# Performance work log

Hardware: AMD Instinct MI355X
Metric: run time of the kernel (lower is better)

Reference implementation:

```python
import jax, jax.numpy as jnp
import numpy as np

B, L, D, N = 32, 512, 512, 8  # batch, length, input_size, num_labels


def setup_inputs() -> dict:
    key = jax.random.key(0)
    k1, k2, k3, k4, k5 = jax.random.split(key, 5)
    scale = 0.02
    return {
        "input_h": jax.random.normal(k1, (B, L, D), dtype=jnp.float32),
        "input_c": jax.random.normal(k2, (B, L, D), dtype=jnp.float32),
        "mask": jnp.ones((B, L), dtype=jnp.float32),
        "U": jax.random.normal(k3, (N, D, D), dtype=jnp.float32) * scale,
        "W_d": jax.random.normal(k4, (N, D), dtype=jnp.float32) * scale,
        "W_e": jax.random.normal(k5, (N, D), dtype=jnp.float32) * scale,
        "b": jnp.zeros((N, 1, 1), dtype=jnp.float32),
    }


def reference(input_h, input_c, mask, U, W_d, W_e, b):
    # Biaffine attention (NeuroNLP2 BiAAttention): head = decoder side, child = encoder side.
    # bilinear term: [b, n, l_head, l_child]
    out = jnp.einsum("bld,nde,bme->bnlm", input_h, U, input_c)
    # linear head term -> broadcast over child axis
    out = out + jnp.einsum("nd,bld->bnl", W_d, input_h)[:, :, :, None]
    # linear child term -> broadcast over head axis
    out = out + jnp.einsum("nd,bmd->bnm", W_e, input_c)[:, :, None, :]
    out = out + b[None]  # bias [n,1,1]
    # mask_d / mask_e multiplicative masking
    out = out * mask[:, None, :, None] * mask[:, None, None, :]
    # -inf on the diagonal (no self-arcs)
    length = out.shape[-1]
    diag = jnp.where(jnp.eye(length, dtype=bool), -jnp.inf, 0.0).astype(out.dtype)
    return out + diag
```

## Files before the change

kernel.cpp:

```cpp
#include <hip/hip_runtime.h>


#define B_ 32
#define L_ 512
#define D_ 512
#define N_ 8
#define MT 64
#define STR 536

using f16x8 = __attribute__((ext_vector_type(8))) _Float16;
using f32x4 = __attribute__((ext_vector_type(4))) float;
using u16x8 = __attribute__((ext_vector_type(8))) unsigned short;

static __device__ __forceinline__ float bf2f(unsigned short h) {
  union { unsigned u; float f; } v; v.u = (unsigned)h << 16; return v.f;
}
static __device__ __forceinline__ float h2f(unsigned short h) {
  _Float16 x; __builtin_memcpy(&x, &h, 2); return (float)x;
}
static __device__ __forceinline__ unsigned short f2h(float f) {
  _Float16 x = (_Float16)f; unsigned short u; __builtin_memcpy(&u, &x, 2); return u;
}

static __device__ __forceinline__ int sniff(const unsigned* mkw) {
  const unsigned w = *mkw;
  if (w == 0x3F800000u) return 0;
  if (w == 0x3C003C00u) return 1;
  if (w == 0x3F803F80u) return 2;
  return 1;
}

static __device__ __forceinline__ float ldscal(const void* base, int idx, int flag) {
  if (flag == 0) return ((const float*)base)[idx];
  const unsigned short u = ((const unsigned short*)base)[idx];
  return (flag == 1) ? h2f(u) : bf2f(u);
}

static __device__ __forceinline__ u16x8 ld8f(const void* base, size_t off, int flag) {
  u16x8 o;
  if (flag == 1) {
    o = *(const u16x8*)((const unsigned short*)base + off);
  } else if (flag == 0) {
    const float4* p = (const float4*)((const float*)base + off);
    float4 a = p[0], bq = p[1];
    o[0]=f2h(a.x); o[1]=f2h(a.y); o[2]=f2h(a.z); o[3]=f2h(a.w);
    o[4]=f2h(bq.x); o[5]=f2h(bq.y); o[6]=f2h(bq.z); o[7]=f2h(bq.w);
  } else {
    u16x8 v = *(const u16x8*)((const unsigned short*)base + off);
#pragma unroll
    for (int j = 0; j < 8; ++j) o[j] = f2h(bf2f(v[j]));
  }
  return o;
}

__global__ __launch_bounds__(256)
void cvt_f16(const void* __restrict__ src, unsigned short* __restrict__ dst, int n8,
             const unsigned* __restrict__ mkw) {
  const int flag = sniff(mkw);
  int i = blockIdx.x * 256 + threadIdx.x;
  const int stride = gridDim.x * 256;
  for (; i < n8; i += stride) {
    u16x8 o = ld8f(src, 8 * (size_t)i, flag);
    *(u16x8*)(dst + 8 * (size_t)i) = o;
  }
}

__global__ __launch_bounds__(256)
void cvt_f16_2(const void* __restrict__ s0, unsigned short* __restrict__ d0, int n0,
               const void* __restrict__ s1, unsigned short* __restrict__ d1, int n1,
               const unsigned* __restrict__ mkw) {
  const int flag = sniff(mkw);
  int i = blockIdx.x * 256 + threadIdx.x;
  const int stride = gridDim.x * 256;
  const int tot = n0 + n1;
  for (; i < tot; i += stride) {
    const void* src; unsigned short* dst; int k;
    if (i < n0) { src = s0; dst = d0; k = i; }
    else        { src = s1; dst = d1; k = i - n0; }
    u16x8 o = ld8f(src, 8 * (size_t)k, flag);
    *(u16x8*)(dst + 8 * (size_t)k) = o;
  }
}

__global__ __launch_bounds__(256)
void prep_c(const void* __restrict__ Cr, unsigned short* __restrict__ Cc,
            float* __restrict__ CTp, const void* __restrict__ We,
            const void* __restrict__ Bia, const unsigned* __restrict__ mkw)
{
  __shared__ float wetab[N_ * 512];
  __shared__ float psum[256 * 9];
  const int flag = sniff(mkw);
  const int tid = threadIdx.x;
  const int b  = blockIdx.x >> 4;
  const int mc = blockIdx.x & 15;

  for (int i = tid; i < N_ * 512; i += 256) wetab[i] = ldscal(We, i, flag);
  __syncthreads();

  const int ml = tid >> 3;
  const int e8 = tid & 7;
  const int m  = mc * 32 + ml;
  const size_t rowOff = ((size_t)b * L_ + m) * D_;

  float pn[N_];
#pragma unroll
  for (int nn = 0; nn < N_; ++nn) pn[nn] = 0.f;

#pragma unroll
  for (int j = 0; j < 8; ++j) {
    const int e0 = (j * 8 + e8) * 8;
    u16x8 v = ld8f(Cr, rowOff + e0, flag);
    *(u16x8*)(Cc + rowOff + e0) = v;
    float cf[8];
#pragma unroll
    for (int k = 0; k < 8; ++k) cf[k] = h2f(v[k]);
#pragma unroll
    for (int nn = 0; nn < N_; ++nn) {
      float s = pn[nn];
#pragma unroll
      for (int k = 0; k < 8; ++k) s += cf[k] * wetab[nn * 512 + e0 + k];
      pn[nn] = s;
    }
  }
#pragma unroll
  for (int nn = 0; nn < N_; ++nn) psum[tid * 9 + nn] = pn[nn];
  __syncthreads();

  {
    const int row = tid >> 3, nn = tid & 7;
    float s = ldscal(Bia, nn, flag);
#pragma unroll
    for (int q = 0; q < 8; ++q) s += psum[(row * 8 + q) * 9 + nn];
    CTp[((size_t)(b * N_ + nn)) * L_ + mc * 32 + row] = s;
  }
}

template <bool CVT, bool CT>
__global__ __launch_bounds__(512)
void biaffine(const unsigned short* __restrict__ Hc, const void* __restrict__ Hr,
              const unsigned short* __restrict__ Cc, const void* __restrict__ Cr,
              const unsigned short* __restrict__ Uc, const void* __restrict__ Ur,
              const float* __restrict__ CTp,
              const void* __restrict__ Mk, const void* __restrict__ Wd,
              const void* __restrict__ We, const void* __restrict__ Bia,
              unsigned short* __restrict__ Out)
{
  __shared__ __align__(16) unsigned short cpb[64 * STR];
  __shared__ float wdv[512], mlv[512];
  __shared__ float wev[512], psum[512];
  __shared__ float colterm[64], mcv[64];

  const int flag = sniff((const unsigned*)Mk);
  const int tid  = threadIdx.x;
  const int wave = tid >> 6;
  const int lane = tid & 63;
  const int quad = lane >> 4;
  const int l16  = lane & 15;

  const int bid = blockIdx.x;
  const int n  = bid & 7;
  const int mt = (bid >> 3) & 7;
  const int b  = bid >> 6;

  const size_t cOff = ((size_t)b * L_ + mt * MT) * D_;
  const size_t hOff = (size_t)b * L_ * D_;
  const size_t uOff = (size_t)n * D_ * D_;

  auto ld8 = [&](const void* base, size_t off) -> u16x8 { return ld8f(base, off, flag); };

  size_t uo[4];
#pragma unroll
  for (int di = 0; di < 4; ++di)
    uo[di] = uOff + (size_t)((4 * wave + di) * 16 + l16) * D_ + quad * 8;

  auto ldU = [&](int di, int s) -> f16x8 {
    if constexpr (CVT) { u16x8 t = ld8(Ur, uo[di] + (size_t)s * 32); return *(f16x8*)&t; }
    else               return *(const f16x8*)(Uc + uo[di] + (size_t)s * 32);
  };

  f16x8 bB[2][4];
#pragma unroll
  for (int di = 0; di < 4; ++di) bB[0][di] = ldU(di, 0);

  {
    const int row = tid >> 3, cb0 = (tid & 7) * 64;
    u16x8 t[8];
#pragma unroll
    for (int j = 0; j < 8; ++j) {
      if constexpr (CVT) t[j] = ld8(Cr, cOff + (size_t)row * D_ + cb0 + j * 8);
      else               t[j] = ((const u16x8*)(Cc + cOff + (size_t)row * D_ + cb0))[j];
    }
    u16x8* dst = (u16x8*)&cpb[row * STR + cb0];
#pragma unroll
    for (int j = 0; j < 8; ++j) dst[j] = t[j];
  }
  wdv[tid] = ldscal(Wd, n * D_ + tid, flag);
  mlv[tid] = ldscal(Mk, b * L_ + tid, flag);
  if (tid < 64) mcv[tid] = ldscal(Mk, b * L_ + mt * MT + tid, flag);
  if constexpr (CT) {
    if (tid < 64) colterm[tid] = CTp[((size_t)(b * N_ + n)) * L_ + mt * MT + tid];
  } else {
    wev[tid] = ldscal(We, n * D_ + tid, flag);
  }
  __syncthreads();

  if constexpr (!CT) {
    {
      const int m = tid >> 3, e0 = (tid & 7) * 64;
      float s = 0.f;
#pragma unroll 8
      for (int e = 0; e < 64; ++e) s += h2f(cpb[m * STR + e0 + e]) * wev[e0 + e];
      psum[tid] = s;
    }
    __syncthreads();
    if (tid < 64) {
      float s = ldscal(Bia, n, flag);
#pragma unroll
      for (int j = 0; j < 8; ++j) s += psum[tid * 8 + j];
      colterm[tid] = s;
    }
  }

  f32x4 acc[4][4];
#pragma unroll
  for (int i = 0; i < 4; ++i)
#pragma unroll
    for (int j = 0; j < 4; ++j) acc[i][j] = (f32x4){0.f, 0.f, 0.f, 0.f};

#pragma unroll
  for (int s = 0; s < 16; ++s) {
    const int cur = s & 1;
    if (s < 15) {
#pragma unroll
      for (int di = 0; di < 4; ++di) bB[cur ^ 1][di] = ldU(di, s + 1);
    }
    f16x8 aF[4];
#pragma unroll
    for (int mi = 0; mi < 4; ++mi)
      aF[mi] = *(const f16x8*)&cpb[(mi * 16 + l16) * STR + s * 32 + quad * 8];
    __builtin_amdgcn_s_setprio(1);
#pragma unroll
    for (int mi = 0; mi < 4; ++mi)
#pragma unroll
      for (int di = 0; di < 4; ++di)
        acc[mi][di] = __builtin_amdgcn_mfma_f32_16x16x32_f16(aF[mi], bB[cur][di], acc[mi][di], 0, 0, 0);
    __builtin_amdgcn_s_setprio(0);
  }

  size_t ho[4];
#pragma unroll
  for (int li = 0; li < 4; ++li)
    ho[li] = hOff + (size_t)((4 * wave + li) * 16 + l16) * D_ + quad * 8;

  auto ldH = [&](int li, int s) -> f16x8 {
    if constexpr (CVT) { u16x8 t = ld8(Hr, ho[li] + (size_t)s * 32); return *(f16x8*)&t; }
    else               return *(const f16x8*)(Hc + ho[li] + (size_t)s * 32);
  };

  f16x8 aB[2][4];
#pragma unroll
  for (int li = 0; li < 4; ++li) aB[0][li] = ldH(li, 0);

  __syncthreads();

#pragma unroll
  for (int di = 0; di < 4; ++di) {
    const int d_g = (4 * wave + di) * 16 + l16;
    const float wd = wdv[d_g];
#pragma unroll
    for (int mi = 0; mi < 4; ++mi)
#pragma unroll
      for (int r = 0; r < 4; ++r) {
        const int m_loc = mi * 16 + quad * 4 + r;
        cpb[m_loc * STR + d_g] = f2h(acc[mi][di][r] + wd);
      }
  }
  __syncthreads();

  f32x4 acc2[4][4];
#pragma unroll
  for (int i = 0; i < 4; ++i)
#pragma unroll
    for (int j = 0; j < 4; ++j) acc2[i][j] = (f32x4){0.f, 0.f, 0.f, 0.f};

#pragma unroll
  for (int s = 0; s < 16; ++s) {
    const int cur = s & 1;
    if (s < 15) {
#pragma unroll
      for (int li = 0; li < 4; ++li) aB[cur ^ 1][li] = ldH(li, s + 1);
    }
    f16x8 bF[4];
#pragma unroll
    for (int mj = 0; mj < 4; ++mj)
      bF[mj] = *(const f16x8*)&cpb[(mj * 16 + l16) * STR + s * 32 + quad * 8];
    __builtin_amdgcn_s_setprio(1);
#pragma unroll
    for (int li = 0; li < 4; ++li)
#pragma unroll
      for (int mj = 0; mj < 4; ++mj)
        acc2[li][mj] = __builtin_amdgcn_mfma_f32_16x16x32_f16(aB[cur][li], bF[mj], acc2[li][mj], 0, 0, 0);
    __builtin_amdgcn_s_setprio(0);
  }

  const size_t outBase = (size_t)(b * N_ + n) * L_ * L_;
#pragma unroll
  for (int mj = 0; mj < 4; ++mj) {
    const int m_loc = mj * 16 + l16;
    const int m_g = mt * MT + m_loc;
    const float cm = colterm[m_loc];
    const float mm = mcv[m_loc];
#pragma unroll
    for (int li = 0; li < 4; ++li)
#pragma unroll
      for (int r = 0; r < 4; ++r) {
        const int l = (4 * wave + li) * 16 + quad * 4 + r;
        const float v = (acc2[li][mj][r] + cm) * (mlv[l] * mm);
        const unsigned short us = (l == m_g) ? (unsigned short)0xFBFFu : f2h(v);
        Out[outBase + (size_t)l * L_ + m_g] = us;
      }
  }
}

extern "C" void kernel_launch(void* const* d_in, const int* in_sizes, int n_in,
                              void* d_out, int out_size, void* d_ws, size_t ws_size,
                              hipStream_t stream) {
  const void* Hr  = d_in[0];
  const void* Cr  = d_in[1];
  const void* Mk  = d_in[2];
  const void* Ur  = d_in[3];
  const void* Wd  = d_in[4];
  const void* We  = d_in[5];
  const void* Bia = d_in[6];
  unsigned short* Out = (unsigned short*)d_out;
  (void)in_sizes; (void)n_in; (void)out_size;

  const size_t nH = (size_t)B_ * L_ * D_;
  const size_t nC = nH;
  const size_t nU = (size_t)N_ * D_ * D_;
  const size_t ctN = (size_t)B_ * N_ * L_;
  const size_t needHalf = (nH + nC + nU) * sizeof(unsigned short);
  const size_t needFull = needHalf + ctN * sizeof(float);

  dim3 grid(B_ * N_ * (L_ / MT));
  dim3 block(512);
  const unsigned* mkw = (const unsigned*)Mk;

  if (ws_size >= needFull) {
    unsigned short* Hc = (unsigned short*)d_ws;
    unsigned short* Cc = Hc + nH;
    unsigned short* Uc = Cc + nC;
    float* CTp = (float*)(Uc + nU);
    prep_c<<<512, 256, 0, stream>>>(Cr, Cc, CTp, We, Bia, mkw);
    cvt_f16_2<<<2048, 256, 0, stream>>>(Hr, Hc, (int)(nH / 8), Ur, Uc, (int)(nU / 8), mkw);
    biaffine<false, true><<<grid, block, 0, stream>>>(Hc, nullptr, Cc, nullptr, Uc, nullptr,
                                                      CTp, Mk, Wd, We, Bia, Out);
  } else if (ws_size >= needHalf) {
    unsigned short* Hc = (unsigned short*)d_ws;
    unsigned short* Cc = Hc + nH;
    unsigned short* Uc = Cc + nC;
    cvt_f16<<<1024, 256, 0, stream>>>(Hr, Hc, (int)(nH / 8), mkw);
    cvt_f16<<<1024, 256, 0, stream>>>(Cr, Cc, (int)(nC / 8), mkw);
    cvt_f16<<<512,  256, 0, stream>>>(Ur, Uc, (int)(nU / 8), mkw);
    biaffine<false, false><<<grid, block, 0, stream>>>(Hc, nullptr, Cc, nullptr, Uc, nullptr,
                                                       nullptr, Mk, Wd, We, Bia, Out);
  } else {
    biaffine<true, false><<<grid, block, 0, stream>>>(nullptr, Hr, nullptr, Cr, nullptr, Ur,
                                                      nullptr, Mk, Wd, We, Bia, Out);
  }
}
```

Baseline: 588.2 us.

## Swap MFMA operand order and XOR-swizzle LDS for vectorized stores

Replaces the padded LDS layout with an XOR-swizzled 512-wide layout and swaps the A/B operands of both MFMA stages. Each lane then holds four consecutive output columns, so both the intermediate LDS write and the global output store become 4-wide vector stores instead of scalar 2-byte stores. This is meant to cut the many uncoalesced scalar global writes of the large fp16 output and to avoid LDS bank conflicts. U and H operand loads are also moved into scoped blocks to shorten register live ranges. The risks are swizzle indexing errors and different register pressure.

New measurement: 575.6 us. -2.1%, faster.

```diff
diff --git a/kernel.cpp b/kernel.cpp
--- a/kernel.cpp
+++ b/kernel.cpp
@@ -6,11 +6,11 @@
 #define D_ 512
 #define N_ 8
 #define MT 64
-#define STR 536
 
 using f16x8 = __attribute__((ext_vector_type(8))) _Float16;
 using f32x4 = __attribute__((ext_vector_type(4))) float;
 using u16x8 = __attribute__((ext_vector_type(8))) unsigned short;
+using u16x4 = __attribute__((ext_vector_type(4))) unsigned short;
 
 static __device__ __forceinline__ float bf2f(unsigned short h) {
   union { unsigned u; float f; } v; v.u = (unsigned)h << 16; return v.f;
@@ -145,7 +145,7 @@
               const void* __restrict__ We, const void* __restrict__ Bia,
               unsigned short* __restrict__ Out)
 {
-  __shared__ __align__(16) unsigned short cpb[64 * STR];
+  __shared__ __align__(16) unsigned short cpb[64 * 512];
   __shared__ float wdv[512], mlv[512];
   __shared__ float wev[512], psum[512];
   __shared__ float colterm[64], mcv[64];
@@ -156,6 +156,7 @@
   const int lane = tid & 63;
   const int quad = lane >> 4;
   const int l16  = lane & 15;
+  const int rsw  = l16 & 7;
 
   const int bid = blockIdx.x;
   const int n  = bid & 7;
@@ -168,31 +169,21 @@
 
   auto ld8 = [&](const void* base, size_t off) -> u16x8 { return ld8f(base, off, flag); };
 
-  size_t uo[4];
-#pragma unroll
-  for (int di = 0; di < 4; ++di)
-    uo[di] = uOff + (size_t)((4 * wave + di) * 16 + l16) * D_ + quad * 8;
-
-  auto ldU = [&](int di, int s) -> f16x8 {
-    if constexpr (CVT) { u16x8 t = ld8(Ur, uo[di] + (size_t)s * 32); return *(f16x8*)&t; }
-    else               return *(const f16x8*)(Uc + uo[di] + (size_t)s * 32);
-  };
-
-  f16x8 bB[2][4];
-#pragma unroll
-  for (int di = 0; di < 4; ++di) bB[0][di] = ldU(di, 0);
-
   {
-    const int row = tid >> 3, cb0 = (tid & 7) * 64;
+    const int srow = (wave << 3) | (lane & 7);
+    const int cg   = lane >> 3;
+    const size_t gbase = cOff + (size_t)srow * D_ + cg * 8;
     u16x8 t[8];
 #pragma unroll
     for (int j = 0; j < 8; ++j) {
-      if constexpr (CVT) t[j] = ld8(Cr, cOff + (size_t)row * D_ + cb0 + j * 8);
-      else               t[j] = ((const u16x8*)(Cc + cOff + (size_t)row * D_ + cb0))[j];
-    }
-    u16x8* dst = (u16x8*)&cpb[row * STR + cb0];
-#pragma unroll
-    for (int j = 0; j < 8; ++j) dst[j] = t[j];
+      if constexpr (CVT) t[j] = ld8(Cr, gbase + (size_t)j * 64);
+      else               t[j] = *(const u16x8*)(Cc + gbase + (size_t)j * 64);
+    }
+    const int sx = srow & 7;
+    unsigned short* rowp = &cpb[srow * 512];
+#pragma unroll
+    for (int j = 0; j < 8; ++j)
+      *(u16x8*)&rowp[((cg + 8 * j) ^ sx) * 8] = t[j];
   }
   wdv[tid] = ldscal(Wd, n * D_ + tid, flag);
   mlv[tid] = ldscal(Mk, b * L_ + tid, flag);
@@ -206,10 +197,15 @@
 
   if constexpr (!CT) {
     {
-      const int m = tid >> 3, e0 = (tid & 7) * 64;
+      const int m = tid >> 3, eg = tid & 7;
       float s = 0.f;
-#pragma unroll 8
-      for (int e = 0; e < 64; ++e) s += h2f(cpb[m * STR + e0 + e]) * wev[e0 + e];
+#pragma unroll
+      for (int k = 0; k < 8; ++k) {
+        const int lc = eg * 8 + k;
+        u16x8 v = *(const u16x8*)&cpb[m * 512 + (lc ^ (m & 7)) * 8];
+#pragma unroll
+        for (int t2 = 0; t2 < 8; ++t2) s += h2f(v[t2]) * wev[lc * 8 + t2];
+      }
       psum[tid] = s;
     }
     __syncthreads();
@@ -227,98 +223,124 @@
 #pragma unroll
     for (int j = 0; j < 4; ++j) acc[i][j] = (f32x4){0.f, 0.f, 0.f, 0.f};
 
-#pragma unroll
-  for (int s = 0; s < 16; ++s) {
-    const int cur = s & 1;
-    if (s < 15) {
-#pragma unroll
-      for (int di = 0; di < 4; ++di) bB[cur ^ 1][di] = ldU(di, s + 1);
-    }
-    f16x8 aF[4];
-#pragma unroll
-    for (int mi = 0; mi < 4; ++mi)
-      aF[mi] = *(const f16x8*)&cpb[(mi * 16 + l16) * STR + s * 32 + quad * 8];
-    __builtin_amdgcn_s_setprio(1);
-#pragma unroll
-    for (int mi = 0; mi < 4; ++mi)
+  {
+    size_t uo[4];
+#pragma unroll
+    for (int di = 0; di < 4; ++di)
+      uo[di] = uOff + (size_t)((4 * wave + di) * 16 + l16) * D_ + quad * 8;
+
+    auto ldU = [&](int di, int s) -> f16x8 {
+      if constexpr (CVT) { u16x8 t = ld8(Ur, uo[di] + (size_t)s * 32); return *(f16x8*)&t; }
+      else               return *(const f16x8*)(Uc + uo[di] + (size_t)s * 32);
+    };
+
+    f16x8 bB[2][4];
+#pragma unroll
+    for (int di = 0; di < 4; ++di) bB[0][di] = ldU(di, 0);
+
+#pragma unroll
+    for (int s = 0; s < 16; ++s) {
+      const int cur = s & 1;
+      if (s < 15) {
+#pragma unroll
+        for (int di = 0; di < 4; ++di) bB[cur ^ 1][di] = ldU(di, s + 1);
+      }
+      f16x8 aF[4];
+#pragma unroll
+      for (int mi = 0; mi < 4; ++mi)
+        aF[mi] = *(const f16x8*)&cpb[(mi * 16 + l16) * 512 + (((s * 4 + quad) ^ rsw) * 8)];
+      __builtin_amdgcn_s_setprio(1);
 #pragma unroll
       for (int di = 0; di < 4; ++di)
-        acc[mi][di] = __builtin_amdgcn_mfma_f32_16x16x32_f16(aF[mi], bB[cur][di], acc[mi][di], 0, 0, 0);
-    __builtin_amdgcn_s_setprio(0);
-  }
-
-  size_t ho[4];
-#pragma unroll
-  for (int li = 0; li < 4; ++li)
-    ho[li] = hOff + (size_t)((4 * wave + li) * 16 + l16) * D_ + quad * 8;
-
-  auto ldH = [&](int li, int s) -> f16x8 {
-    if constexpr (CVT) { u16x8 t = ld8(Hr, ho[li] + (size_t)s * 32); return *(f16x8*)&t; }
-    else               return *(const f16x8*)(Hc + ho[li] + (size_t)s * 32);
-  };
-
-  f16x8 aB[2][4];
-#pragma unroll
-  for (int li = 0; li < 4; ++li) aB[0][li] = ldH(li, 0);
-
+#pragma unroll
+        for (int mi = 0; mi < 4; ++mi)
+          acc[di][mi] = __builtin_amdgcn_mfma_f32_16x16x32_f16(bB[cur][di], aF[mi], acc[di][mi], 0, 0, 0);
+      __builtin_amdgcn_s_setprio(0);
+    }
+  }
   __syncthreads();
 
 #pragma unroll
   for (int di = 0; di < 4; ++di) {
-    const int d_g = (4 * wave + di) * 16 + l16;
-    const float wd = wdv[d_g];
-#pragma unroll
-    for (int mi = 0; mi < 4; ++mi)
+    const int d0 = (4 * wave + di) * 16 + quad * 4;
+    const float4 w4 = *(const float4*)&wdv[d0];
+    const float wd[4] = {w4.x, w4.y, w4.z, w4.w};
+    const int chunkb = d0 >> 3;
+    const int dlo = d0 & 7;
+#pragma unroll
+    for (int mi = 0; mi < 4; ++mi) {
+      const int m_loc = mi * 16 + l16;
+      u16x4 o;
+#pragma unroll
+      for (int r = 0; r < 4; ++r) o[r] = f2h(acc[di][mi][r] + wd[r]);
+      *(u16x4*)&cpb[m_loc * 512 + ((chunkb ^ rsw) * 8) + dlo] = o;
+    }
+  }
+  __syncthreads();
+
+  f32x4 acc2[4][4];
+#pragma unroll
+  for (int i = 0; i < 4; ++i)
+#pragma unroll
+    for (int j = 0; j < 4; ++j) acc2[i][j] = (f32x4){0.f, 0.f, 0.f, 0.f};
+
+  {
+    size_t ho[4];
+#pragma unroll
+    for (int li = 0; li < 4; ++li)
+      ho[li] = hOff + (size_t)((4 * wave + li) * 16 + l16) * D_ + quad * 8;
+
+    auto ldH = [&](int li, int s) -> f16x8 {
+      if constexpr (CVT) { u16x8 t = ld8(Hr, ho[li] + (size_t)s * 32); return *(f16x8*)&t; }
+      else               return *(const f16x8*)(Hc + ho[li] + (size_t)s * 32);
+    };
+
+    f16x8 aB[2][4];
+#pragma unroll
+    for (int li = 0; li < 4; ++li) aB[0][li] = ldH(li, 0);
+
+#pragma unroll
+    for (int s = 0; s < 16; ++s) {
+      const int cur = s & 1;
+      if (s < 15) {
+#pragma unroll
+        for (int li = 0; li < 4; ++li) aB[cur ^ 1][li] = ldH(li, s + 1);
+      }
+      f16x8 bF[4];
+#pragma unroll
+      for (int mj = 0; mj < 4; ++mj)
+        bF[mj] = *(const f16x8*)&cpb[(mj * 16 + l16) * 512 + (((s * 4 + quad) ^ rsw) * 8)];
+      __builtin_amdgcn_s_setprio(1);
+#pragma unroll
+      for (int mj = 0; mj < 4; ++mj)
+#pragma unroll
+        for (int li = 0; li < 4; ++li)
+          acc2[mj][li] = __builtin_amdgcn_mfma_f32_16x16x32_f16(bF[mj], aB[cur][li], acc2[mj][li], 0, 0, 0);
+      __builtin_amdgcn_s_setprio(0);
+    }
+  }
+
+  const size_t outBase = (size_t)(b * N_ + n) * L_ * L_;
+#pragma unroll
+  for (int li = 0; li < 4; ++li) {
+    const int l = (4 * wave + li) * 16 + l16;
+    const float ml = mlv[l];
+#pragma unroll
+    for (int mj = 0; mj < 4; ++mj) {
+      const int mb = mj * 16 + quad * 4;
+      const float4 c4 = *(const float4*)&colterm[mb];
+      const float4 m4 = *(const float4*)&mcv[mb];
+      const int m_g0 = mt * MT + mb;
+      const float ct[4] = {c4.x, c4.y, c4.z, c4.w};
+      const float mm[4] = {m4.x, m4.y, m4.z, m4.w};
+      u16x4 o;
 #pragma unroll
       for (int r = 0; r < 4; ++r) {
-        const int m_loc = mi * 16 + quad * 4 + r;
-        cpb[m_loc * STR + d_g] = f2h(acc[mi][di][r] + wd);
+        const float v = (acc2[mj][li][r] + ct[r]) * (ml * mm[r]);
+        o[r] = (l == m_g0 + r) ? (unsigned short)0xFBFFu : f2h(v);
       }
-  }
-  __syncthreads();
-
-  f32x4 acc2[4][4];
-#pragma unroll
-  for (int i = 0; i < 4; ++i)
-#pragma unroll
-    for (int j = 0; j < 4; ++j) acc2[i][j] = (f32x4){0.f, 0.f, 0.f, 0.f};
-
-#pragma unroll
-  for (int s = 0; s < 16; ++s) {
-    const int cur = s & 1;
-    if (s < 15) {
-#pragma unroll
-      for (int li = 0; li < 4; ++li) aB[cur ^ 1][li] = ldH(li, s + 1);
-    }
-    f16x8 bF[4];
-#pragma unroll
-    for (int mj = 0; mj < 4; ++mj)
-      bF[mj] = *(const f16x8*)&cpb[(mj * 16 + l16) * STR + s * 32 + quad * 8];
-    __builtin_amdgcn_s_setprio(1);
-#pragma unroll
-    for (int li = 0; li < 4; ++li)
-#pragma unroll
-      for (int mj = 0; mj < 4; ++mj)
-        acc2[li][mj] = __builtin_amdgcn_mfma_f32_16x16x32_f16(aB[cur][li], bF[mj], acc2[li][mj], 0, 0, 0);
-    __builtin_amdgcn_s_setprio(0);
-  }
-
-  const size_t outBase = (size_t)(b * N_ + n) * L_ * L_;
-#pragma unroll
-  for (int mj = 0; mj < 4; ++mj) {
-    const int m_loc = mj * 16 + l16;
-    const int m_g = mt * MT + m_loc;
-    const float cm = colterm[m_loc];
-    const float mm = mcv[m_loc];
-#pragma unroll
-    for (int li = 0; li < 4; ++li)
-#pragma unroll
-      for (int r = 0; r < 4; ++r) {
-        const int l = (4 * wave + li) * 16 + quad * 4 + r;
-        const float v = (acc2[li][mj][r] + cm) * (mlv[l] * mm);
-        const unsigned short us = (l == m_g) ? (unsigned short)0xFBFFu : f2h(v);
-        Out[outBase + (size_t)l * L_ + m_g] = us;
-      }
+      *(u16x4*)&Out[outBase + (size_t)l * L_ + m_g0] = o;
+    }
   }
 }
 
```
